# Kernel tuning notes

Measured on AMD Instinct MI355X. Metric: run time of the kernel, lower is better.

Reference implementation:

```python
import jax, jax.numpy as jnp
import numpy as np
from jax import lax

NUM_MASKS = 100
NUM_CLASSES = 81  # 80 + 1
KERNEL_DIM = 256
BIAS_PRIOR = float(-np.log((1 - 0.01) / 0.01))


def setup_inputs() -> dict:
    key = jax.random.key(0)
    ks = jax.random.split(key, 12)
    B, C, H, W = 4, 256, 160, 160
    D = C  # expand_dim = in_channels * num_groups
    inp = {
        "features": jax.random.normal(ks[0], (B, C, H, W), jnp.float32),
        # iam_conv: Conv2d(C, num_masks, 3, padding=1)
        "w_iam": jax.random.normal(ks[1], (NUM_MASKS, C, 3, 3), jnp.float32) * 0.01,
        "b_iam": jnp.full((NUM_MASKS,), BIAS_PRIOR, jnp.float32),
        "softmax_bias": jnp.ones((1,), jnp.float32),
        # fc: Linear(D, D), xavier-ish
        "w_fc": jax.random.normal(ks[2], (D, D), jnp.float32) * (1.0 / np.sqrt(D)),
        "b_fc": jnp.zeros((D,), jnp.float32),
        "w_cls": jax.random.normal(ks[3], (NUM_CLASSES, D), jnp.float32) * 0.01,
        "b_cls": jnp.full((NUM_CLASSES,), BIAS_PRIOR, jnp.float32),
        "w_ker": jax.random.normal(ks[4], (KERNEL_DIM, D), jnp.float32) * 0.01,
        "b_ker": jnp.zeros((KERNEL_DIM,), jnp.float32),
        "w_obj": jax.random.normal(ks[5], (1, D), jnp.float32) * (1.0 / np.sqrt(D)),
        "b_obj": jnp.zeros((1,), jnp.float32),
        "w_box": jax.random.normal(ks[6], (4, D), jnp.float32) * 0.01,
        "b_box": jnp.zeros((4,), jnp.float32),
    }
    return inp


def reference(features, w_iam, b_iam, softmax_bias, w_fc, b_fc,
              w_cls, b_cls, w_ker, b_ker, w_obj, b_obj, w_box, b_box):
    B, C, H, W = features.shape
    # conv score map: (B, num_masks, H, W)
    iam = lax.conv_general_dilated(
        features, w_iam, window_strides=(1, 1), padding="SAME",
        dimension_numbers=("NCHW", "OIHW", "NCHW")) + b_iam[None, :, None, None]
    # num_groups == 1: single group iam
    iam_flat = iam.reshape(B, NUM_MASKS, H * W)
    # softmax over HW with learned scalar bias (bias shifts uniformly -> no-op math-wise but kept faithful)
    iam_prob = jax.nn.softmax(iam_flat + softmax_bias[0], axis=-1)  # (B, M, HW)
    # spatial attention pooling: bmm(prob, feats^T) -> (B, M, C)
    inst = jnp.einsum("bmp,bcp->bmc", iam_prob, features.reshape(B, C, H * W))
    # prev_inst_features is None -> skip fc_fuse
    inst = jax.nn.relu(inst @ w_fc.T + b_fc)
    pred_logits = inst @ w_cls.T + b_cls
    pred_kernel = inst @ w_ker.T + b_ker
    pred_scores = inst @ w_obj.T + b_obj
    pred_bboxes = inst @ w_box.T + b_box
    return (pred_logits, pred_kernel, pred_scores, pred_bboxes, iam, inst)
```

## Files before the change

### kernel.cpp

```cpp
#include <hip/hip_runtime.h>
#include <hip/hip_bf16.h>

typedef __attribute__((ext_vector_type(8))) short bf16x8;
typedef __attribute__((ext_vector_type(4))) float f32x4;

#define HW_ 25600
#define HP_ 162
#define WP_ 162

__device__ __forceinline__ unsigned short f2bf(float f) {
    union { float f; unsigned u; } x; x.f = f;
    unsigned r = x.u + 0x7FFFu + ((x.u >> 16) & 1u);
    return (unsigned short)(r >> 16);
}

typedef const __attribute__((address_space(1))) unsigned int* gas_t;
typedef __attribute__((address_space(3))) unsigned int* las_t;
__device__ __forceinline__ void gl_lds16(const void* g, void* l) {
    __builtin_amdgcn_global_load_lds((gas_t)g, (las_t)l, 16, 0, 0);
}

__global__ __launch_bounds__(256) void k_prepw(const float* __restrict__ w_iam,
                                               unsigned short* __restrict__ wp) {
    int idx = blockIdx.x * 256 + threadIdx.x;
    if (idx >= 36 * 8192) return;
    int stage = idx >> 13;
    int r8 = idx & 8191;
    int m = r8 >> 6, cl = r8 & 63;
    int tap = stage >> 2, cc = stage & 3;
    int jj = (cl >> 3) ^ (m & 7);
    int c = cc * 64 + jj * 8 + (cl & 7);
    int dy = tap / 3, dx = tap - dy * 3;
    float v = (m < 100) ? w_iam[((m * 256 + c) * 3 + dy) * 3 + dx] : 0.f;
    wp[idx] = f2bf(v);
}

__global__ __launch_bounds__(256) void k_border(unsigned short* __restrict__ fpad) {
    int idx = blockIdx.x * 256 + threadIdx.x;
    const int perb = 164864;
    if (idx >= 4 * perb) return;
    int b = idx / perb;
    int r = idx - b * perb;
    int hp, wpp, c;
    if (r < 82944) {
        hp = (r < 41472) ? 0 : 161;
        int r2 = r % 41472;
        wpp = r2 >> 8; c = r2 & 255;
    } else {
        r -= 82944;
        wpp = (r < 40960) ? 0 : 161;
        int r2 = r % 40960;
        hp = 1 + (r2 >> 8); c = r2 & 255;
    }
    fpad[((b * HP_ + hp) * WP_ + wpp) * 256 + c] = 0;
}

__global__ __launch_bounds__(256) void k_convert(const float* __restrict__ feat,
                                                 unsigned short* __restrict__ fpad) {
    int bid = blockIdx.x;
    int b = bid / 640;
    int h = (bid >> 2) % 160;
    int c0 = (bid & 3) * 64;
    __shared__ float tile[64][161];
    int t = threadIdx.x;
    const float* src = feat + ((long)(b * 256 + c0) * 160 + h) * 160;
    for (int s = 0; s < 40; ++s) {
        int q = t + s * 256;
        int ci = q / 160;
        int w = q - ci * 160;
        tile[ci][w] = src[(long)ci * HW_ + w];
    }
    __syncthreads();
    int co = (t & 7) * 8, wq = t >> 3;
    unsigned short* dst = fpad + ((long)(b * HP_ + h + 1) * WP_ + 1) * 256 + c0 + co;
    for (int wp = 0; wp < 5; ++wp) {
        int w = wq + wp * 32;
        bf16x8 v;
        #pragma unroll
        for (int j = 0; j < 8; ++j) v[j] = (short)f2bf(tile[co + j][w]);
        *(bf16x8*)(dst + (long)w * 256) = v;
    }
}

__global__ __launch_bounds__(256) void k_conv(const unsigned short* __restrict__ fpad,
                                              const unsigned short* __restrict__ wprep,
                                              const float* __restrict__ b_iam,
                                              float* __restrict__ iam) {
    int bid = blockIdx.x;
    bid = (bid & 7) * 100 + (bid >> 3);
    int b = bid / 200;
    int p0 = (bid % 200) * 128;
    int tid = threadIdx.x;
    int lane = tid & 63, wid = tid >> 6;

    __shared__ __align__(16) unsigned short As[2][8192];
    __shared__ __align__(16) unsigned short Bs[2][8192];

    const unsigned short* fb = fpad + (long)b * HP_ * WP_ * 256;
    const unsigned short* gB[4];
    int csw = (((tid & 7) ^ ((tid >> 3) & 7)) << 3);
    #pragma unroll
    for (int rnd = 0; rnd < 4; ++rnd) {
        int r = (tid >> 3) + rnd * 32;
        int p = p0 + r;
        int h = p / 160, w = p - h * 160;
        gB[rnd] = fb + ((long)h * WP_ + w) * 256 + csw;
    }
    const unsigned short* gA0 = wprep + (tid << 3);

    f32x4 acc[7][2];
    #pragma unroll
    for (int i = 0; i < 7; ++i)
        #pragma unroll
        for (int j = 0; j < 2; ++j)
            #pragma unroll
            for (int k = 0; k < 4; ++k) acc[i][j][k] = 0.f;

    int arow = lane & 15;
    int cs0 = ((((lane >> 4) ^ (lane & 7))) << 3);
    int cs1 = cs0 ^ 32;

    auto issue = [&](int s, int bi) {
        int tap = s >> 2, cc = s & 3;
        int dy = tap / 3, dx = tap - dy * 3;
        long boff = ((long)dy * WP_ + dx) * 256 + cc * 64;
        const unsigned short* ga = gA0 + ((long)s << 13);
        char* Ad = (char*)As[bi];
        char* Bd = (char*)Bs[bi];
        #pragma unroll
        for (int rnd = 0; rnd < 4; ++rnd) {
            gl_lds16(ga + (rnd << 11), Ad + (wid << 10) + (rnd << 12));
            gl_lds16(gB[rnd] + boff,   Bd + (wid << 10) + (rnd << 12));
        }
    };

    auto compute = [&](int bi) {
        const unsigned short* Ab = As[bi];
        const unsigned short* Bb = Bs[bi];
        #pragma unroll
        for (int kk = 0; kk < 2; ++kk) {
            int co = kk ? cs1 : cs0;
            bf16x8 af[7], bfv[2];
            #pragma unroll
            for (int mf = 0; mf < 7; ++mf)
                af[mf] = *(const bf16x8*)(Ab + (mf * 16 + arow) * 64 + co);
            #pragma unroll
            for (int nf = 0; nf < 2; ++nf)
                bfv[nf] = *(const bf16x8*)(Bb + (wid * 32 + nf * 16 + arow) * 64 + co);
            #pragma unroll
            for (int mf = 0; mf < 7; ++mf)
                #pragma unroll
                for (int nf = 0; nf < 2; ++nf)
                    acc[mf][nf] = __builtin_amdgcn_mfma_f32_16x16x32_bf16(
                        af[mf], bfv[nf], acc[mf][nf], 0, 0, 0);
        }
    };

    issue(0, 0);
    issue(1, 1);
    for (int s = 0; s < 35; ++s) {
        asm volatile("s_waitcnt vmcnt(8)" ::: "memory");
        __builtin_amdgcn_sched_barrier(0);
        __builtin_amdgcn_s_barrier();
        __builtin_amdgcn_sched_barrier(0);
        compute(s & 1);
        __builtin_amdgcn_sched_barrier(0);
        __builtin_amdgcn_s_barrier();
        __builtin_amdgcn_sched_barrier(0);
        if (s < 34) issue(s + 2, s & 1);
    }
    asm volatile("s_waitcnt vmcnt(0)" ::: "memory");
    __builtin_amdgcn_sched_barrier(0);
    __builtin_amdgcn_s_barrier();
    __builtin_amdgcn_sched_barrier(0);
    compute(1);

    float* dst = iam + (long)b * 100 * HW_;
    #pragma unroll
    for (int mf = 0; mf < 7; ++mf)
        #pragma unroll
        for (int nf = 0; nf < 2; ++nf) {
            int p = p0 + wid * 32 + nf * 16 + (lane & 15);
            int m0 = mf * 16 + ((lane >> 4) << 2);
            #pragma unroll
            for (int j = 0; j < 4; ++j) {
                int m = m0 + j;
                if (m < 100) dst[(long)m * HW_ + p] = acc[mf][nf][j] + b_iam[m];
            }
        }
}

__global__ __launch_bounds__(256, 2) void k_pool(const float* __restrict__ feat,
                                                 const float* __restrict__ iam,
                                                 float* __restrict__ partials,
                                                 float* __restrict__ psum) {
    int bid = blockIdx.x;
    int b = bid / 50;
    int slice = bid - b * 50;
    int p0 = slice * 512;
    int tid = threadIdx.x, lane = tid & 63, wq = tid >> 6;

    __shared__ __align__(16) unsigned short A[128 * 72];
    __shared__ __align__(16) unsigned short Bl[256 * 72];
    __shared__ float sums[128];
    if (tid < 128) sums[tid] = 0.f;
    __syncthreads();

    f32x4 acc[7][4];
    #pragma unroll
    for (int i = 0; i < 7; ++i)
        #pragma unroll
        for (int j = 0; j < 4; ++j)
            #pragma unroll
            for (int k = 0; k < 4; ++k) acc[i][j][k] = 0.f;

    int kgrp = (lane >> 4) << 3;

    for (int ks = 0; ks < 8; ++ks) {
        int k0 = p0 + ks * 64;
        for (int s = 0; s < 4; ++s) {
            int q = tid + s * 256;
            int mi = q >> 3, j0 = (q & 7) * 8;
            bf16x8 o;
            if (mi < 100) {
                const float4* sp4 = (const float4*)(iam + (long)(b * 100 + mi) * HW_ + k0 + j0);
                float4 v0 = sp4[0], v1 = sp4[1];
                float xv[8] = {v0.x, v0.y, v0.z, v0.w, v1.x, v1.y, v1.z, v1.w};
                float ls = 0.f;
                #pragma unroll
                for (int j = 0; j < 8; ++j) {
                    float e = __expf(xv[j]);
                    o[j] = (short)f2bf(e);
                    ls += e;
                }
                atomicAdd(&sums[mi], ls);
            } else {
                #pragma unroll
                for (int j = 0; j < 8; ++j) o[j] = 0;
            }
            *(bf16x8*)(A + mi * 72 + j0) = o;
        }
        for (int s = 0; s < 8; ++s) {
            int q = tid + s * 256;
            int ci = q >> 3, j0 = (q & 7) * 8;
            const float4* sp4 = (const float4*)(feat + (long)(b * 256 + ci) * HW_ + k0 + j0);
            float4 v0 = sp4[0], v1 = sp4[1];
            float xv[8] = {v0.x, v0.y, v0.z, v0.w, v1.x, v1.y, v1.z, v1.w};
            bf16x8 o;
            #pragma unroll
            for (int j = 0; j < 8; ++j) o[j] = (short)f2bf(xv[j]);
            *(bf16x8*)(Bl + ci * 72 + j0) = o;
        }
        __syncthreads();
        #pragma unroll
        for (int kk = 0; kk < 64; kk += 32) {
            bf16x8 af[7], bfv[4];
            #pragma unroll
            for (int mf = 0; mf < 7; ++mf)
                af[mf] = *(const bf16x8*)(A + (mf * 16 + (lane & 15)) * 72 + kk + kgrp);
            #pragma unroll
            for (int nf = 0; nf < 4; ++nf)
                bfv[nf] = *(const bf16x8*)(Bl + (wq * 64 + nf * 16 + (lane & 15)) * 72 + kk + kgrp);
            #pragma unroll
            for (int mf = 0; mf < 7; ++mf)
                #pragma unroll
                for (int nf = 0; nf < 4; ++nf)
                    acc[mf][nf] = __builtin_amdgcn_mfma_f32_16x16x32_bf16(
                        af[mf], bfv[nf], acc[mf][nf], 0, 0, 0);
        }
        __syncthreads();
    }
    if (tid < 100) psum[(long)(b * 50 + slice) * 112 + tid] = sums[tid];
    float* dst = partials + (long)(b * 50 + slice) * 112 * 256;
    #pragma unroll
    for (int mf = 0; mf < 7; ++mf)
        #pragma unroll
        for (int nf = 0; nf < 4; ++nf) {
            int m0 = mf * 16 + ((lane >> 4) << 2);
            int c  = wq * 64 + nf * 16 + (lane & 15);
            #pragma unroll
            for (int j = 0; j < 4; ++j)
                dst[(long)(m0 + j) * 256 + c] = acc[mf][nf][j];
        }
}

__global__ __launch_bounds__(256) void k_redpool(const float* __restrict__ partials,
                                                 const float* __restrict__ psum,
                                                 float* __restrict__ inst_pool) {
    int bid = blockIdx.x;
    int b = bid / 100, m = bid - b * 100;
    int c = threadIdx.x;
    float s = 0.f, d = 0.f;
    for (int sl = 0; sl < 50; ++sl) {
        s += partials[((long)(b * 50 + sl) * 112 + m) * 256 + c];
        d += psum[(long)(b * 50 + sl) * 112 + m];
    }
    inst_pool[(long)bid * 256 + c] = s / d;
}

__global__ __launch_bounds__(256) void k_fc(const float* __restrict__ inst_pool,
                                            const float* __restrict__ w_fc, const float* __restrict__ b_fc,
                                            const float* __restrict__ w_cls, const float* __restrict__ b_cls,
                                            const float* __restrict__ w_ker, const float* __restrict__ b_ker,
                                            const float* __restrict__ w_obj, const float* __restrict__ b_obj,
                                            const float* __restrict__ w_box, const float* __restrict__ b_box,
                                            float* __restrict__ out) {
    int r = blockIdx.x;
    int t = threadIdx.x;
    __shared__ float row[256];
    __shared__ float inst_s[256];
    row[t] = inst_pool[(long)r * 256 + t];
    __syncthreads();
    {
        float acc = b_fc[t];
        const float4* wv = (const float4*)(w_fc + (long)t * 256);
        for (int c = 0; c < 64; ++c) {
            float4 w4 = wv[c];
            acc += w4.x * row[c * 4] + w4.y * row[c * 4 + 1] + w4.z * row[c * 4 + 2] + w4.w * row[c * 4 + 3];
        }
        acc = fmaxf(acc, 0.f);
        inst_s[t] = acc;
        out[10376800 + (long)r * 256 + t] = acc;
    }
    __syncthreads();
    {
        float acc = b_ker[t];
        const float4* wv = (const float4*)(w_ker + (long)t * 256);
        for (int c = 0; c < 64; ++c) {
            float4 w4 = wv[c];
            acc += w4.x * inst_s[c * 4] + w4.y * inst_s[c * 4 + 1] + w4.z * inst_s[c * 4 + 2] + w4.w * inst_s[c * 4 + 3];
        }
        out[32400 + (long)r * 256 + t] = acc;
    }
    if (t < 81) {
        float acc = b_cls[t];
        const float4* wv = (const float4*)(w_cls + (long)t * 256);
        for (int c = 0; c < 64; ++c) {
            float4 w4 = wv[c];
            acc += w4.x * inst_s[c * 4] + w4.y * inst_s[c * 4 + 1] + w4.z * inst_s[c * 4 + 2] + w4.w * inst_s[c * 4 + 3];
        }
        out[(long)r * 81 + t] = acc;
    }
    if (t == 0) {
        float acc = b_obj[0];
        for (int c = 0; c < 256; ++c) acc += w_obj[c] * inst_s[c];
        out[134800 + r] = acc;
    }
    if (t >= 1 && t < 5) {
        int j = t - 1;
        float acc = b_box[j];
        for (int c = 0; c < 256; ++c) acc += w_box[j * 256 + c] * inst_s[c];
        out[135200 + (long)r * 4 + j] = acc;
    }
}

extern "C" void kernel_launch(void* const* d_in, const int* in_sizes, int n_in,
                              void* d_out, int out_size, void* d_ws, size_t ws_size,
                              hipStream_t stream) {
    const float* feat  = (const float*)d_in[0];
    const float* w_iam = (const float*)d_in[1];
    const float* b_iam = (const float*)d_in[2];
    const float* w_fc  = (const float*)d_in[4];
    const float* b_fc  = (const float*)d_in[5];
    const float* w_cls = (const float*)d_in[6];
    const float* b_cls = (const float*)d_in[7];
    const float* w_ker = (const float*)d_in[8];
    const float* b_ker = (const float*)d_in[9];
    const float* w_obj = (const float*)d_in[10];
    const float* b_obj = (const float*)d_in[11];
    const float* w_box = (const float*)d_in[12];
    const float* b_box = (const float*)d_in[13];
    float* out = (float*)d_out;

    char* ws = (char*)d_ws;
    unsigned short* fpad  = (unsigned short*)ws;
    unsigned short* wprep = (unsigned short*)(ws + 53747712);
    float* partials  = (float*)ws;
    float* psum      = (float*)(ws + 22937600);
    float* inst_pool = (float*)(ws + 23027200);

    float* iam = out + 136800;

    k_prepw  <<<dim3(1152), dim3(256), 0, stream>>>(w_iam, wprep);
    k_border <<<dim3(2576), dim3(256), 0, stream>>>(fpad);
    k_convert<<<dim3(2560), dim3(256), 0, stream>>>(feat, fpad);
    k_conv   <<<dim3(800),  dim3(256), 0, stream>>>(fpad, wprep, b_iam, iam);
    k_pool   <<<dim3(200),  dim3(256), 0, stream>>>(feat, iam, partials, psum);
    k_redpool<<<dim3(400),  dim3(256), 0, stream>>>(partials, psum, inst_pool);
    k_fc     <<<dim3(400),  dim3(256), 0, stream>>>(inst_pool, w_fc, b_fc, w_cls, b_cls,
                                                    w_ker, b_ker, w_obj, b_obj, w_box, b_box, out);
}
```

Measured before the change: 201.5 us.

## Retile conv GEMM to 2x2 wave layout with K=32 stages; split pooling finer

The conv implicit GEMM moves from each wave owning 112x32 outputs to a 2x2 wave grid of 64x64 tiles, with 32-channel K chunks across 72 stages. It uses smaller LDS buffers, targets 3 blocks per CU, raises wave priority during the MFMA bursts, and restructures the prefetch loop. Weight prep and border zeroing are merged into a single launch, and the feature convert uses float4 loads. Pooling is split into 400 blocks of 256 pixels for more parallelism, at the cost of twice as many partials to reduce.

```diff
diff --git a/kernel.cpp b/kernel.cpp
--- a/kernel.cpp
+++ b/kernel.cpp
@@ -20,39 +20,40 @@
     __builtin_amdgcn_global_load_lds((gas_t)g, (las_t)l, 16, 0, 0);
 }
 
-__global__ __launch_bounds__(256) void k_prepw(const float* __restrict__ w_iam,
-                                               unsigned short* __restrict__ wp) {
-    int idx = blockIdx.x * 256 + threadIdx.x;
-    if (idx >= 36 * 8192) return;
-    int stage = idx >> 13;
-    int r8 = idx & 8191;
-    int m = r8 >> 6, cl = r8 & 63;
-    int tap = stage >> 2, cc = stage & 3;
-    int jj = (cl >> 3) ^ (m & 7);
-    int c = cc * 64 + jj * 8 + (cl & 7);
-    int dy = tap / 3, dx = tap - dy * 3;
-    float v = (m < 100) ? w_iam[((m * 256 + c) * 3 + dy) * 3 + dx] : 0.f;
-    wp[idx] = f2bf(v);
-}
-
-__global__ __launch_bounds__(256) void k_border(unsigned short* __restrict__ fpad) {
-    int idx = blockIdx.x * 256 + threadIdx.x;
-    const int perb = 164864;
-    if (idx >= 4 * perb) return;
-    int b = idx / perb;
-    int r = idx - b * perb;
-    int hp, wpp, c;
-    if (r < 82944) {
-        hp = (r < 41472) ? 0 : 161;
-        int r2 = r % 41472;
-        wpp = r2 >> 8; c = r2 & 255;
+__global__ __launch_bounds__(256) void k_prep(const float* __restrict__ w_iam,
+                                              unsigned short* __restrict__ wp,
+                                              unsigned short* __restrict__ fpad) {
+    int bid = blockIdx.x;
+    if (bid < 1152) {
+        int idx = bid * 256 + threadIdx.x;
+        int stage = idx >> 12;
+        int r = idx & 4095;
+        int m = r >> 5, cl = r & 31;
+        int tap = stage >> 3, kc = stage & 7;
+        int jj = (cl >> 3) ^ ((m >> 1) & 3);
+        int c = kc * 32 + jj * 8 + (cl & 7);
+        int dy = (tap * 11) >> 5, dx = tap - dy * 3;
+        float v = (m < 100) ? w_iam[((m * 256 + c) * 3 + dy) * 3 + dx] : 0.f;
+        wp[idx] = f2bf(v);
     } else {
-        r -= 82944;
-        wpp = (r < 40960) ? 0 : 161;
-        int r2 = r % 40960;
-        hp = 1 + (r2 >> 8); c = r2 & 255;
-    }
-    fpad[((b * HP_ + hp) * WP_ + wpp) * 256 + c] = 0;
+        int idx = (bid - 1152) * 256 + threadIdx.x;
+        const int perb = 164864;
+        if (idx >= 4 * perb) return;
+        int b = idx / perb;
+        int r = idx - b * perb;
+        int hp, wpp, c;
+        if (r < 82944) {
+            hp = (r < 41472) ? 0 : 161;
+            int r2 = r % 41472;
+            wpp = r2 >> 8; c = r2 & 255;
+        } else {
+            r -= 82944;
+            wpp = (r < 40960) ? 0 : 161;
+            int r2 = r % 40960;
+            hp = 1 + (r2 >> 8); c = r2 & 255;
+        }
+        fpad[((b * HP_ + hp) * WP_ + wpp) * 256 + c] = 0;
+    }
 }
 
 __global__ __launch_bounds__(256) void k_convert(const float* __restrict__ feat,
@@ -63,16 +64,22 @@
     int c0 = (bid & 3) * 64;
     __shared__ float tile[64][161];
     int t = threadIdx.x;
-    const float* src = feat + ((long)(b * 256 + c0) * 160 + h) * 160;
-    for (int s = 0; s < 40; ++s) {
+    const float4* src4 = (const float4*)(feat + ((long)(b * 256 + c0) * 160 + h) * 160);
+    #pragma unroll
+    for (int s = 0; s < 10; ++s) {
         int q = t + s * 256;
-        int ci = q / 160;
-        int w = q - ci * 160;
-        tile[ci][w] = src[(long)ci * HW_ + w];
+        int ci = q / 40;
+        int w4 = q - ci * 40;
+        float4 v = src4[(long)ci * 6400 + w4];
+        tile[ci][w4 * 4 + 0] = v.x;
+        tile[ci][w4 * 4 + 1] = v.y;
+        tile[ci][w4 * 4 + 2] = v.z;
+        tile[ci][w4 * 4 + 3] = v.w;
     }
     __syncthreads();
     int co = (t & 7) * 8, wq = t >> 3;
     unsigned short* dst = fpad + ((long)(b * HP_ + h + 1) * WP_ + 1) * 256 + c0 + co;
+    #pragma unroll
     for (int wp = 0; wp < 5; ++wp) {
         int w = wq + wp * 32;
         bf16x8 v;
@@ -82,84 +89,84 @@
     }
 }
 
-__global__ __launch_bounds__(256) void k_conv(const unsigned short* __restrict__ fpad,
-                                              const unsigned short* __restrict__ wprep,
-                                              const float* __restrict__ b_iam,
-                                              float* __restrict__ iam) {
+__global__ __launch_bounds__(256, 3) void k_conv(const unsigned short* __restrict__ fpad,
+                                                 const unsigned short* __restrict__ wprep,
+                                                 const float* __restrict__ b_iam,
+                                                 float* __restrict__ iam) {
     int bid = blockIdx.x;
     bid = (bid & 7) * 100 + (bid >> 3);
     int b = bid / 200;
     int p0 = (bid % 200) * 128;
     int tid = threadIdx.x;
     int lane = tid & 63, wid = tid >> 6;
-
-    __shared__ __align__(16) unsigned short As[2][8192];
-    __shared__ __align__(16) unsigned short Bs[2][8192];
+    int wr = wid >> 1, wc = wid & 1;
+
+    __shared__ __align__(16) unsigned short As[2][4096];
+    __shared__ __align__(16) unsigned short Bs[2][4096];
 
     const unsigned short* fb = fpad + (long)b * HP_ * WP_ * 256;
-    const unsigned short* gB[4];
-    int csw = (((tid & 7) ^ ((tid >> 3) & 7)) << 3);
-    #pragma unroll
-    for (int rnd = 0; rnd < 4; ++rnd) {
-        int r = (tid >> 3) + rnd * 32;
-        int p = p0 + r;
-        int h = p / 160, w = p - h * 160;
-        gB[rnd] = fb + ((long)h * WP_ + w) * 256 + csw;
-    }
-    const unsigned short* gA0 = wprep + (tid << 3);
-
-    f32x4 acc[7][2];
-    #pragma unroll
-    for (int i = 0; i < 7; ++i)
-        #pragma unroll
-        for (int j = 0; j < 2; ++j)
+    const unsigned short* gBsrc[2];
+    {
+        int swz = ((lane & 3) ^ ((lane >> 3) & 3)) * 8;
+        #pragma unroll
+        for (int i = 0; i < 2; ++i) {
+            int pr = i * 64 + wid * 16 + (lane >> 2);
+            int p = p0 + pr;
+            int h = p / 160, w = p - h * 160;
+            gBsrc[i] = fb + ((long)h * WP_ + w) * 256 + swz;
+        }
+    }
+    const unsigned short* gA0 = wprep + (wid << 9) + (lane << 3);
+
+    f32x4 acc[4][4];
+    #pragma unroll
+    for (int i = 0; i < 4; ++i)
+        #pragma unroll
+        for (int j = 0; j < 4; ++j)
             #pragma unroll
             for (int k = 0; k < 4; ++k) acc[i][j][k] = 0.f;
 
-    int arow = lane & 15;
-    int cs0 = ((((lane >> 4) ^ (lane & 7))) << 3);
-    int cs1 = cs0 ^ 32;
+    int chB   = (((lane >> 4) ^ ((lane >> 1) & 3)) << 4);
+    int aBase = (wr << 12) + ((lane & 15) << 6) + chB;
+    int bBase = (wc << 12) + ((lane & 15) << 6) + chB;
 
     auto issue = [&](int s, int bi) {
-        int tap = s >> 2, cc = s & 3;
-        int dy = tap / 3, dx = tap - dy * 3;
-        long boff = ((long)dy * WP_ + dx) * 256 + cc * 64;
-        const unsigned short* ga = gA0 + ((long)s << 13);
-        char* Ad = (char*)As[bi];
-        char* Bd = (char*)Bs[bi];
-        #pragma unroll
-        for (int rnd = 0; rnd < 4; ++rnd) {
-            gl_lds16(ga + (rnd << 11), Ad + (wid << 10) + (rnd << 12));
-            gl_lds16(gB[rnd] + boff,   Bd + (wid << 10) + (rnd << 12));
-        }
+        int tap = s >> 3, kc = s & 7;
+        int dy = (tap * 11) >> 5, dx = tap - dy * 3;
+        long boff = ((long)dy * WP_ + dx) * 256 + kc * 32;
+        const unsigned short* ga = gA0 + ((long)s << 12);
+        char* Ad = (char*)As[bi] + (wid << 10);
+        char* Bd = (char*)Bs[bi] + (wid << 10);
+        gl_lds16(ga, Ad);
+        gl_lds16(ga + 2048, Ad + 4096);
+        gl_lds16(gBsrc[0] + boff, Bd);
+        gl_lds16(gBsrc[1] + boff, Bd + 4096);
     };
 
     auto compute = [&](int bi) {
-        const unsigned short* Ab = As[bi];
-        const unsigned short* Bb = Bs[bi];
-        #pragma unroll
-        for (int kk = 0; kk < 2; ++kk) {
-            int co = kk ? cs1 : cs0;
-            bf16x8 af[7], bfv[2];
-            #pragma unroll
-            for (int mf = 0; mf < 7; ++mf)
-                af[mf] = *(const bf16x8*)(Ab + (mf * 16 + arow) * 64 + co);
-            #pragma unroll
-            for (int nf = 0; nf < 2; ++nf)
-                bfv[nf] = *(const bf16x8*)(Bb + (wid * 32 + nf * 16 + arow) * 64 + co);
-            #pragma unroll
-            for (int mf = 0; mf < 7; ++mf)
-                #pragma unroll
-                for (int nf = 0; nf < 2; ++nf)
-                    acc[mf][nf] = __builtin_amdgcn_mfma_f32_16x16x32_bf16(
-                        af[mf], bfv[nf], acc[mf][nf], 0, 0, 0);
-        }
+        const char* Ab = (const char*)As[bi];
+        const char* Bb = (const char*)Bs[bi];
+        bf16x8 af[4], bfv[4];
+        #pragma unroll
+        for (int mf = 0; mf < 4; ++mf)
+            af[mf] = *(const bf16x8*)(Ab + aBase + (mf << 10));
+        #pragma unroll
+        for (int nf = 0; nf < 4; ++nf)
+            bfv[nf] = *(const bf16x8*)(Bb + bBase + (nf << 10));
+        __builtin_amdgcn_s_setprio(1);
+        #pragma unroll
+        for (int mf = 0; mf < 4; ++mf)
+            #pragma unroll
+            for (int nf = 0; nf < 4; ++nf)
+                acc[mf][nf] = __builtin_amdgcn_mfma_f32_16x16x32_bf16(
+                    af[mf], bfv[nf], acc[mf][nf], 0, 0, 0);
+        __builtin_amdgcn_s_setprio(0);
     };
 
     issue(0, 0);
-    issue(1, 1);
-    for (int s = 0; s < 35; ++s) {
-        asm volatile("s_waitcnt vmcnt(8)" ::: "memory");
+    for (int s = 0; s < 71; ++s) {
+        issue(s + 1, (s + 1) & 1);
+        asm volatile("s_waitcnt vmcnt(4)" ::: "memory");
         __builtin_amdgcn_sched_barrier(0);
         __builtin_amdgcn_s_barrier();
         __builtin_amdgcn_sched_barrier(0);
@@ -167,7 +174,6 @@
         __builtin_amdgcn_sched_barrier(0);
         __builtin_amdgcn_s_barrier();
         __builtin_amdgcn_sched_barrier(0);
-        if (s < 34) issue(s + 2, s & 1);
     }
     asm volatile("s_waitcnt vmcnt(0)" ::: "memory");
     __builtin_amdgcn_sched_barrier(0);
@@ -177,11 +183,11 @@
 
     float* dst = iam + (long)b * 100 * HW_;
     #pragma unroll
-    for (int mf = 0; mf < 7; ++mf)
-        #pragma unroll
-        for (int nf = 0; nf < 2; ++nf) {
-            int p = p0 + wid * 32 + nf * 16 + (lane & 15);
-            int m0 = mf * 16 + ((lane >> 4) << 2);
+    for (int mf = 0; mf < 4; ++mf)
+        #pragma unroll
+        for (int nf = 0; nf < 4; ++nf) {
+            int p = p0 + wc * 64 + nf * 16 + (lane & 15);
+            int m0 = wr * 64 + mf * 16 + ((lane >> 4) << 2);
             #pragma unroll
             for (int j = 0; j < 4; ++j) {
                 int m = m0 + j;
@@ -195,9 +201,9 @@
                                                  float* __restrict__ partials,
                                                  float* __restrict__ psum) {
     int bid = blockIdx.x;
-    int b = bid / 50;
-    int slice = bid - b * 50;
-    int p0 = slice * 512;
+    int b = bid / 100;
+    int slice = bid - b * 100;
+    int p0 = slice * 256;
     int tid = threadIdx.x, lane = tid & 63, wq = tid >> 6;
 
     __shared__ __align__(16) unsigned short A[128 * 72];
@@ -216,7 +222,7 @@
 
     int kgrp = (lane >> 4) << 3;
 
-    for (int ks = 0; ks < 8; ++ks) {
+    for (int ks = 0; ks < 4; ++ks) {
         int k0 = p0 + ks * 64;
         for (int s = 0; s < 4; ++s) {
             int q = tid + s * 256;
@@ -270,8 +276,8 @@
         }
         __syncthreads();
     }
-    if (tid < 100) psum[(long)(b * 50 + slice) * 112 + tid] = sums[tid];
-    float* dst = partials + (long)(b * 50 + slice) * 112 * 256;
+    if (tid < 100) psum[(long)bid * 112 + tid] = sums[tid];
+    float* dst = partials + (long)bid * 112 * 256;
     #pragma unroll
     for (int mf = 0; mf < 7; ++mf)
         #pragma unroll
@@ -291,9 +297,9 @@
     int b = bid / 100, m = bid - b * 100;
     int c = threadIdx.x;
     float s = 0.f, d = 0.f;
-    for (int sl = 0; sl < 50; ++sl) {
-        s += partials[((long)(b * 50 + sl) * 112 + m) * 256 + c];
-        d += psum[(long)(b * 50 + sl) * 112 + m];
+    for (int sl = 0; sl < 100; ++sl) {
+        s += partials[((long)(b * 100 + sl) * 112 + m) * 256 + c];
+        d += psum[(long)(b * 100 + sl) * 112 + m];
     }
     inst_pool[(long)bid * 256 + c] = s / d;
 }
@@ -376,16 +382,15 @@
     unsigned short* fpad  = (unsigned short*)ws;
     unsigned short* wprep = (unsigned short*)(ws + 53747712);
     float* partials  = (float*)ws;
-    float* psum      = (float*)(ws + 22937600);
-    float* inst_pool = (float*)(ws + 23027200);
+    float* psum      = (float*)(ws + 45875200);
+    float* inst_pool = (float*)(ws + 46054400);
 
     float* iam = out + 136800;
 
-    k_prepw  <<<dim3(1152), dim3(256), 0, stream>>>(w_iam, wprep);
-    k_border <<<dim3(2576), dim3(256), 0, stream>>>(fpad);
+    k_prep   <<<dim3(3728), dim3(256), 0, stream>>>(w_iam, wprep, fpad);
     k_convert<<<dim3(2560), dim3(256), 0, stream>>>(feat, fpad);
     k_conv   <<<dim3(800),  dim3(256), 0, stream>>>(fpad, wprep, b_iam, iam);
-    k_pool   <<<dim3(200),  dim3(256), 0, stream>>>(feat, iam, partials, psum);
+    k_pool   <<<dim3(400),  dim3(256), 0, stream>>>(feat, iam, partials, psum);
     k_redpool<<<dim3(400),  dim3(256), 0, stream>>>(partials, psum, inst_pool);
     k_fc     <<<dim3(400),  dim3(256), 0, stream>>>(inst_pool, w_fc, b_fc, w_cls, b_cls,
                                                     w_ker, b_ker, w_obj, b_obj, w_box, b_box, out);
```

Result: slower. 211.7 us (+5.0%).
